# Performance work log

Hardware: AMD Instinct MI355X
Metric: run time of the kernel (lower is better)

## Reference

```python
import jax, jax.numpy as jnp
import numpy as np

D_MODEL = 768
NUM_HEADS = 12
HEAD_DIM = D_MODEL // NUM_HEADS

def setup_inputs() -> dict:
    key = jax.random.key(0)
    ks = jax.random.split(key, 7)
    B, S = 2, 4096
    q = jax.random.normal(ks[0], (B, S, D_MODEL), dtype=jnp.float32)
    k = jax.random.normal(ks[1], (B, S, D_MODEL), dtype=jnp.float32)
    v = jax.random.normal(ks[2], (B, S, D_MODEL), dtype=jnp.float32)
    # nn.Linear(d, d, bias=False): weight [out, in], y = x @ W.T
    s = 1.0 / np.sqrt(D_MODEL)
    W_q = jax.random.uniform(ks[3], (D_MODEL, D_MODEL), jnp.float32, -s, s)
    W_k = jax.random.uniform(ks[4], (D_MODEL, D_MODEL), jnp.float32, -s, s)
    W_v = jax.random.uniform(ks[5], (D_MODEL, D_MODEL), jnp.float32, -s, s)
    W_o = jax.random.uniform(ks[6], (D_MODEL, D_MODEL), jnp.float32, -s, s)
    return {"query": q, "key": k, "value": v,
            "W_q": W_q, "W_k": W_k, "W_v": W_v, "W_o": W_o}

def reference(query, key, value, W_q, W_k, W_v, W_o):
    B, S, _ = query.shape
    H, Dh = NUM_HEADS, HEAD_DIM
    scale = np.sqrt(Dh).astype(np.float32)

    def proj(x, W):  # x [B,S,D] -> [B,H,S,Dh]
        y = jnp.einsum('bsd,ed->bse', x, W)
        return y.reshape(B, S, H, Dh).transpose(0, 2, 1, 3)

    Q = proj(query, W_q)
    K = proj(key, W_k)
    V = proj(value, W_v)
    scores = jnp.einsum('bhqd,bhkd->bhqk', Q, K) / scale
    attn = jax.nn.softmax(scores, axis=-1)  # dropout p=0 -> identity (eval)
    out = jnp.einsum('bhqk,bhkd->bhqd', attn, V)
    out = out.transpose(0, 2, 1, 3).reshape(B, S, H * Dh)
    return jnp.einsum('bsd,ed->bse', out, W_o)
```

## Files before the change

### kernel.cpp

```cpp
#include <hip/hip_runtime.h>

#define D_MODEL 768
#define S_LEN   4096
#define NHEAD   12
#define HDIM    64
#define BATCH   2
#define M_ROWS  (BATCH * S_LEN)

typedef __bf16    bf16x8 __attribute__((ext_vector_type(8)));
typedef float     f32x4  __attribute__((ext_vector_type(4)));
typedef float     f32x16 __attribute__((ext_vector_type(16)));
typedef unsigned  u32x4  __attribute__((ext_vector_type(4)));

#define QSCALE 0.18033688011f

__device__ __forceinline__ unsigned int bfb(float x) {
    return (unsigned int)__builtin_bit_cast(unsigned short, (__bf16)x);
}

__device__ __forceinline__ unsigned cvtpk(float lo, float hi) {
    unsigned r;
    asm("v_cvt_pk_bf16_f32 %0, %1, %2" : "=v"(r) : "v"(lo), "v"(hi));
    return r;
}

#if !__has_builtin(__builtin_amdgcn_exp2f)
extern "C" __device__ float __ocml_native_exp2_f32(float);
#endif
__device__ __forceinline__ float fexp2(float x) {
#if __has_builtin(__builtin_amdgcn_exp2f)
    return __builtin_amdgcn_exp2f(x);
#else
    return __ocml_native_exp2_f32(x);
#endif
}

__device__ __forceinline__ void gload16(const void* g, const void* l) {
    __builtin_amdgcn_global_load_lds(
        (const __attribute__((address_space(1))) unsigned int*)g,
        (__attribute__((address_space(3))) unsigned int*)l, 16, 0, 0);
}

#define MFMA16(a, b, c) __builtin_amdgcn_mfma_f32_16x16x32_bf16(a, b, c, 0, 0, 0)
#define MFMA32(a, b, c) __builtin_amdgcn_mfma_f32_32x32x16_bf16(a, b, c, 0, 0, 0)

__global__ __launch_bounds__(256)
void cvt_bf16(const float* __restrict__ s0, const float* __restrict__ s1,
              const float* __restrict__ s2, const float* __restrict__ s3,
              __bf16* __restrict__ d0, __bf16* __restrict__ d1,
              __bf16* __restrict__ d2, __bf16* __restrict__ d3, int n) {
    const int z = blockIdx.y;
    const float* s = z == 0 ? s0 : z == 1 ? s1 : z == 2 ? s2 : s3;
    __bf16*      d = z == 0 ? d0 : z == 1 ? d1 : z == 2 ? d2 : d3;
    const size_t i = ((size_t)blockIdx.x * 256 + threadIdx.x) * 8;
    if (i >= (size_t)n) return;
    float4 a = *(const float4*)(s + i);
    float4 b = *(const float4*)(s + i + 4);
    bf16x8 o;
    o[0] = (__bf16)a.x; o[1] = (__bf16)a.y; o[2] = (__bf16)a.z; o[3] = (__bf16)a.w;
    o[4] = (__bf16)b.x; o[5] = (__bf16)b.y; o[6] = (__bf16)b.z; o[7] = (__bf16)b.w;
    *(bf16x8*)(d + i) = o;
}

__global__ __launch_bounds__(256)
void mm_qkv(const __bf16* __restrict__ X0, const __bf16* __restrict__ X1,
            const __bf16* __restrict__ X2, const __bf16* __restrict__ W0,
            const __bf16* __restrict__ W1, const __bf16* __restrict__ W2,
            __bf16* __restrict__ C0q, __bf16* __restrict__ C1k,
            __bf16* __restrict__ C2v) {
    __shared__ __align__(16) char lds[24576];
    const int z = blockIdx.z;
    const __bf16* Xb = z == 0 ? X0 : z == 1 ? X1 : X2;
    const __bf16* Wb = z == 0 ? W0 : z == 1 ? W1 : W2;

    const int t    = threadIdx.x;
    const int w    = t >> 6;
    const int wr   = w >> 1, wc = w & 1;
    const int lane = t & 63;
    const int q15  = lane & 15;
    const int g    = lane >> 4;
    const int n0   = blockIdx.x * 64;
    const int m0   = blockIdx.y * 128;

    f32x4 acc[4][2];
#pragma unroll
    for (int i = 0; i < 4; i++)
#pragma unroll
        for (int j = 0; j < 2; j++) acc[i][j] = (f32x4){0.f, 0.f, 0.f, 0.f};

    const int crow = lane >> 3;
    const int xcol = ((lane & 7) ^ crow) << 3;

    for (int k0 = 0; k0 < D_MODEL; k0 += 64) {
        __syncthreads();
#pragma unroll
        for (int j = 0; j < 4; j++) {
            const int c = 4 * w + j;
            gload16(Xb + (size_t)(m0 + 8 * c + crow) * D_MODEL + k0 + xcol,
                    lds + c * 1024);
        }
#pragma unroll
        for (int j = 0; j < 2; j++) {
            const int c = 2 * w + j;
            gload16(Wb + (size_t)(n0 + 8 * c + crow) * D_MODEL + k0 + xcol,
                    lds + 16384 + c * 1024);
        }
        __syncthreads();

#pragma unroll
        for (int kc = 0; kc < 2; kc++) {
            bf16x8 xa[4], wf[2];
#pragma unroll
            for (int mi = 0; mi < 4; mi++) {
                const int r = wr * 64 + mi * 16 + q15;
                xa[mi] = *(const bf16x8*)(lds + r * 128 +
                    ((64 * kc + 16 * g) ^ ((r & 7) << 4)));
            }
#pragma unroll
            for (int nj = 0; nj < 2; nj++) {
                const int r = wc * 32 + nj * 16 + q15;
                wf[nj] = *(const bf16x8*)(lds + 16384 + r * 128 +
                    ((64 * kc + 16 * g) ^ ((r & 7) << 4)));
            }
#pragma unroll
            for (int mi = 0; mi < 4; mi++)
#pragma unroll
                for (int nj = 0; nj < 2; nj++)
                    acc[mi][nj] = MFMA16(xa[mi], wf[nj], acc[mi][nj]);
        }
    }

#pragma unroll
    for (int mi = 0; mi < 4; mi++) {
#pragma unroll
        for (int nj = 0; nj < 2; nj++) {
            const int n  = n0 + wc * 32 + nj * 16 + q15;
            const int mb = m0 + wr * 64 + mi * 16 + 4 * g;
            const int h = n >> 6, dh = n & 63;
            if (z == 0) {
#pragma unroll
                for (int r = 0; r < 4; r++) {
                    const int m = mb + r, b = m >> 12, s = m & 4095;
                    C0q[(((size_t)(b * NHEAD + h)) * S_LEN + s) * HDIM + dh] =
                        (__bf16)(acc[mi][nj][r] * QSCALE);
                }
            } else if (z == 1) {
#pragma unroll
                for (int r = 0; r < 4; r++) {
                    const int m = mb + r, b = m >> 12, s = m & 4095;
                    C1k[(((size_t)(b * NHEAD + h)) * S_LEN + s) * HDIM + dh] =
                        (__bf16)acc[mi][nj][r];
                }
            } else {
                const int b = mb >> 12, s = mb & 4095;
                uint2 pk;
                pk.x = bfb(acc[mi][nj][0]) | (bfb(acc[mi][nj][1]) << 16);
                pk.y = bfb(acc[mi][nj][2]) | (bfb(acc[mi][nj][3]) << 16);
                *(uint2*)(C2v +
                    (((size_t)(b * NHEAD + h)) * HDIM + dh) * S_LEN + s) = pk;
            }
        }
    }
}

__global__ __launch_bounds__(256)
void mm_out(const __bf16* __restrict__ Xb, const __bf16* __restrict__ Wb,
            float* __restrict__ C0) {
    __shared__ __align__(16) char lds[24576];
    const int t    = threadIdx.x;
    const int w    = t >> 6;
    const int wr   = w >> 1, wc = w & 1;
    const int lane = t & 63;
    const int q15  = lane & 15;
    const int g    = lane >> 4;
    const int n0   = blockIdx.x * 64;
    const int m0   = blockIdx.y * 128;

    f32x4 acc[4][2];
#pragma unroll
    for (int i = 0; i < 4; i++)
#pragma unroll
        for (int j = 0; j < 2; j++) acc[i][j] = (f32x4){0.f, 0.f, 0.f, 0.f};

    const int crow = lane >> 3;
    const int xcol = ((lane & 7) ^ crow) << 3;

    for (int k0 = 0; k0 < D_MODEL; k0 += 64) {
        __syncthreads();
#pragma unroll
        for (int j = 0; j < 4; j++) {
            const int c = 4 * w + j;
            gload16(Xb + (size_t)(m0 + 8 * c + crow) * D_MODEL + k0 + xcol,
                    lds + c * 1024);
        }
#pragma unroll
        for (int j = 0; j < 2; j++) {
            const int c = 2 * w + j;
            gload16(Wb + (size_t)(n0 + 8 * c + crow) * D_MODEL + k0 + xcol,
                    lds + 16384 + c * 1024);
        }
        __syncthreads();

#pragma unroll
        for (int kc = 0; kc < 2; kc++) {
            bf16x8 xa[4], wf[2];
#pragma unroll
            for (int mi = 0; mi < 4; mi++) {
                const int r = wr * 64 + mi * 16 + q15;
                xa[mi] = *(const bf16x8*)(lds + r * 128 +
                    ((64 * kc + 16 * g) ^ ((r & 7) << 4)));
            }
#pragma unroll
            for (int nj = 0; nj < 2; nj++) {
                const int r = wc * 32 + nj * 16 + q15;
                wf[nj] = *(const bf16x8*)(lds + 16384 + r * 128 +
                    ((64 * kc + 16 * g) ^ ((r & 7) << 4)));
            }
#pragma unroll
            for (int mi = 0; mi < 4; mi++)
#pragma unroll
                for (int nj = 0; nj < 2; nj++)
                    acc[mi][nj] = MFMA16(xa[mi], wf[nj], acc[mi][nj]);
        }
    }

#pragma unroll
    for (int mi = 0; mi < 4; mi++)
#pragma unroll
        for (int nj = 0; nj < 2; nj++) {
            const int n  = n0 + wc * 32 + nj * 16 + q15;
            const int mb = m0 + wr * 64 + mi * 16 + 4 * g;
#pragma unroll
            for (int r = 0; r < 4; r++)
                C0[(size_t)(mb + r) * D_MODEL + n] = acc[mi][nj][r];
        }
}

__global__ __launch_bounds__(256, 2)
void flash_attn(const __bf16* __restrict__ Qb, const char* __restrict__ Kb,
                const char* __restrict__ Vtb, __bf16* __restrict__ Ab) {
    __shared__ __align__(16) char lds[32768];
    const int t    = threadIdx.x;
    const int w    = t >> 6;
    const int lane = t & 63;
    const int q31  = lane & 31;
    const int hl   = lane >> 5;
    const int swz  = (q31 & 7) << 4;

    const int bid = blockIdx.x;
    const int sb  = (bid & 7) * 96 + (bid >> 3);
    const int bh  = sb >> 5;
    const int qi  = sb & 31;
    const int b   = bh / NHEAD, h = bh % NHEAD;
    const int q0  = qi * 128 + w * 32;

    const char* kbase = Kb  + (size_t)bh * (S_LEN * HDIM * 2);
    const char* vbase = Vtb + (size_t)bh * (HDIM * S_LEN * 2);

    bf16x8 qf[4];
#pragma unroll
    for (int kc = 0; kc < 4; kc++)
        qf[kc] = *(const bf16x8*)(Qb +
            ((size_t)bh * S_LEN + q0 + q31) * HDIM + kc * 16 + hl * 8);

    const bf16x8 onesv = __builtin_bit_cast(bf16x8,
        (u32x4){0x3F803F80u, 0x3F803F80u, 0x3F803F80u, 0x3F803F80u});

    f32x16 o[2], ol;
#pragma unroll
    for (int mt = 0; mt < 2; mt++)
#pragma unroll
        for (int r = 0; r < 16; r++) o[mt][r] = 0.f;
#pragma unroll
    for (int r = 0; r < 16; r++) ol[r] = 0.f;

    const int crow = lane >> 3;
    const int scb  = ((lane & 7) << 4) ^ (crow << 4);

#define STAGE(BASE, KT)                                                        \
    {                                                                          \
        _Pragma("unroll")                                                      \
        for (int j = 0; j < 2; j++) {                                          \
            const int c = 2 * w + j;                                           \
            gload16(kbase + (size_t)((KT) * 64 + c * 8 + crow) * 128 + scb,    \
                    (BASE) + c * 1024);                                        \
            gload16(vbase + (size_t)(c * 8 + crow) * (S_LEN * 2) +             \
                        (size_t)(KT) * 128 + scb,                              \
                    (BASE) + 8192 + c * 1024);                                 \
        }                                                                      \
    }

#define COMPUTE(BASE)                                                          \
    {                                                                          \
        const char* Kt = (BASE);                                               \
        const char* Vt = (BASE) + 8192;                                        \
        f32x16 sA[2];                                                          \
        _Pragma("unroll")                                                      \
        for (int mt = 0; mt < 2; mt++)                                         \
            _Pragma("unroll")                                                  \
            for (int r = 0; r < 16; r++) sA[mt][r] = 0.f;                      \
        __builtin_amdgcn_s_setprio(1);                                         \
        _Pragma("unroll")                                                      \
        for (int kc = 0; kc < 4; kc++) {                                       \
            bf16x8 kf0 = *(const bf16x8*)(Kt + q31 * 128 +                     \
                                          ((32 * kc + 16 * hl) ^ swz));        \
            bf16x8 kf1 = *(const bf16x8*)(Kt + (32 + q31) * 128 +              \
                                          ((32 * kc + 16 * hl) ^ swz));        \
            sA[0] = MFMA32(kf0, qf[kc], sA[0]);                                \
            sA[1] = MFMA32(kf1, qf[kc], sA[1]);                                \
        }                                                                      \
        __builtin_amdgcn_s_setprio(0);                                         \
        _Pragma("unroll")                                                      \
        for (int mt = 0; mt < 2; mt++)                                         \
            _Pragma("unroll")                                                  \
            for (int r = 0; r < 16; r++) sA[mt][r] = fexp2(sA[mt][r]);         \
        u32x4 pf[4];                                                           \
        _Pragma("unroll")                                                      \
        for (int mt = 0; mt < 2; mt++)                                         \
            _Pragma("unroll")                                                  \
            for (int kvc = 0; kvc < 2; kvc++) {                                \
                unsigned w0 = cvtpk(sA[mt][8*kvc+0], sA[mt][8*kvc+1]);         \
                unsigned w1 = cvtpk(sA[mt][8*kvc+2], sA[mt][8*kvc+3]);         \
                unsigned w2 = cvtpk(sA[mt][8*kvc+4], sA[mt][8*kvc+5]);         \
                unsigned w3 = cvtpk(sA[mt][8*kvc+6], sA[mt][8*kvc+7]);         \
                asm volatile("v_permlane32_swap_b32 %0, %1"                    \
                             : "+v"(w0), "+v"(w2));                            \
                asm volatile("v_permlane32_swap_b32 %0, %1"                    \
                             : "+v"(w1), "+v"(w3));                            \
                pf[mt * 2 + kvc] = (u32x4){w0, w1, w2, w3};                    \
            }                                                                  \
        __builtin_amdgcn_s_setprio(1);                                         \
        _Pragma("unroll")                                                      \
        for (int ks = 0; ks < 4; ks++)                                         \
            ol = MFMA32(onesv, __builtin_bit_cast(bf16x8, pf[ks]), ol);        \
        _Pragma("unroll")                                                      \
        for (int mtd = 0; mtd < 2; mtd++)                                      \
            _Pragma("unroll")                                                  \
            for (int ks = 0; ks < 4; ks++) {                                   \
                bf16x8 vf = *(const bf16x8*)(Vt + (32 * mtd + q31) * 128 +     \
                                             ((32 * ks + 16 * hl) ^ swz));     \
                o[mtd] = MFMA32(vf,                                            \
                    __builtin_bit_cast(bf16x8, pf[ks]), o[mtd]);               \
            }                                                                  \
        __builtin_amdgcn_s_setprio(0);                                         \
    }

    STAGE(lds, 0);
    __syncthreads();
#pragma unroll 1
    for (int kt = 0; kt < S_LEN / 64; kt += 2) {
        STAGE(lds + 16384, kt + 1);
        COMPUTE(lds);
        __syncthreads();
        if (kt + 2 < S_LEN / 64) STAGE(lds, kt + 2);
        COMPUTE(lds + 16384);
        __syncthreads();
    }
#undef STAGE
#undef COMPUTE

    const float inv  = 1.0f / ol[0];
    const int   qrow = q0 + q31;
    __bf16* orow = Ab + ((size_t)b * S_LEN + qrow) * D_MODEL + h * HDIM;
#pragma unroll
    for (int mtd = 0; mtd < 2; mtd++)
#pragma unroll
        for (int rg = 0; rg < 4; rg++) {
            const int d0 = 32 * mtd + 8 * rg + 4 * hl;
            uint2 pk;
            pk.x = cvtpk(o[mtd][rg * 4 + 0] * inv, o[mtd][rg * 4 + 1] * inv);
            pk.y = cvtpk(o[mtd][rg * 4 + 2] * inv, o[mtd][rg * 4 + 3] * inv);
            *(uint2*)(orow + d0) = pk;
        }
}

extern "C" void kernel_launch(void* const* d_in, const int* in_sizes, int n_in,
                              void* d_out, int out_size, void* d_ws, size_t ws_size,
                              hipStream_t stream) {
    const float* q  = (const float*)d_in[0];
    const float* k  = (const float*)d_in[1];
    const float* v  = (const float*)d_in[2];
    const float* Wq = (const float*)d_in[3];
    const float* Wk = (const float*)d_in[4];
    const float* Wv = (const float*)d_in[5];
    const float* Wo = (const float*)d_in[6];
    float* out = (float*)d_out;

    const size_t per = (size_t)M_ROWS * D_MODEL;
    const size_t wsz = (size_t)D_MODEL * D_MODEL;
    __bf16* ws  = (__bf16*)d_ws;
    __bf16* qb  = ws;
    __bf16* kb  = qb  + per;
    __bf16* vb  = kb  + per;
    __bf16* Wqb = vb  + per;
    __bf16* Wkb = Wqb + wsz;
    __bf16* Wvb = Wkb + wsz;
    __bf16* Wob = Wvb + wsz;
    __bf16* Qhi = Wob + wsz;
    __bf16* Kbb = Qhi + per;
    __bf16* Vtb = Kbb + per;

    cvt_bf16<<<dim3((int)(per / 2048), 3), 256, 0, stream>>>(
        q, k, v, nullptr, qb, kb, vb, nullptr, (int)per);
    cvt_bf16<<<dim3((int)(wsz / 2048), 4), 256, 0, stream>>>(
        Wq, Wk, Wv, Wo, Wqb, Wkb, Wvb, Wob, (int)wsz);

    dim3 mmg(D_MODEL / 64, M_ROWS / 128, 3);
    mm_qkv<<<mmg, 256, 0, stream>>>(qb, kb, vb, Wqb, Wkb, Wvb, Qhi, Kbb, Vtb);

    flash_attn<<<768, 256, 0, stream>>>(Qhi, (const char*)Kbb,
                                        (const char*)Vtb, qb );

    dim3 mmo(D_MODEL / 64, M_ROWS / 128);
    mm_out<<<mmo, 256, 0, stream>>>(qb, Wob, out);
}
```

Before: 214.9 us.

## Split attention waves over query and key halves, reduce partials via LDS

Each wave now owns 64 query rows and half of every 64-key tile, so each K and V fragment read from LDS feeds two MFMAs instead of one. The row-sum MFMA against a ones vector is replaced by VALU summation of the exponentials plus a cross-half shuffle. The two key-half partial outputs and sums are combined through LDS at the end. Launch bounds rise to 3 blocks per CU, which tightens the register budget against the now larger per-wave accumulator state and may cause spills.

```diff
diff --git a/kernel.cpp b/kernel.cpp
--- a/kernel.cpp
+++ b/kernel.cpp
@@ -236,12 +236,14 @@
         }
 }
 
-__global__ __launch_bounds__(256, 2)
+__global__ __launch_bounds__(256, 3)
 void flash_attn(const __bf16* __restrict__ Qb, const char* __restrict__ Kb,
                 const char* __restrict__ Vtb, __bf16* __restrict__ Ab) {
-    __shared__ __align__(16) char lds[32768];
+    __shared__ __align__(16) char lds[33792];
     const int t    = threadIdx.x;
     const int w    = t >> 6;
+    const int qh   = w >> 1;
+    const int kh   = w & 1;
     const int lane = t & 63;
     const int q31  = lane & 31;
     const int hl   = lane >> 5;
@@ -252,27 +254,28 @@
     const int bh  = sb >> 5;
     const int qi  = sb & 31;
     const int b   = bh / NHEAD, h = bh % NHEAD;
-    const int q0  = qi * 128 + w * 32;
+    const int q0  = qi * 128;
 
     const char* kbase = Kb  + (size_t)bh * (S_LEN * HDIM * 2);
     const char* vbase = Vtb + (size_t)bh * (HDIM * S_LEN * 2);
 
-    bf16x8 qf[4];
-#pragma unroll
-    for (int kc = 0; kc < 4; kc++)
-        qf[kc] = *(const bf16x8*)(Qb +
-            ((size_t)bh * S_LEN + q0 + q31) * HDIM + kc * 16 + hl * 8);
-
-    const bf16x8 onesv = __builtin_bit_cast(bf16x8,
-        (u32x4){0x3F803F80u, 0x3F803F80u, 0x3F803F80u, 0x3F803F80u});
-
-    f32x16 o[2], ol;
-#pragma unroll
-    for (int mt = 0; mt < 2; mt++)
-#pragma unroll
-        for (int r = 0; r < 16; r++) o[mt][r] = 0.f;
-#pragma unroll
-    for (int r = 0; r < 16; r++) ol[r] = 0.f;
+    bf16x8 qf[2][4];
+#pragma unroll
+    for (int qb = 0; qb < 2; qb++)
+#pragma unroll
+        for (int kc = 0; kc < 4; kc++)
+            qf[qb][kc] = *(const bf16x8*)(Qb +
+                ((size_t)bh * S_LEN + q0 + 64 * qh + 32 * qb + q31) * HDIM +
+                kc * 16 + hl * 8);
+
+    f32x16 o[2][2];
+#pragma unroll
+    for (int qb = 0; qb < 2; qb++)
+#pragma unroll
+        for (int mtd = 0; mtd < 2; mtd++)
+#pragma unroll
+            for (int r = 0; r < 16; r++) o[qb][mtd][r] = 0.f;
+    float lrun[2] = {0.f, 0.f};
 
     const int crow = lane >> 3;
     const int scb  = ((lane & 7) << 4) ^ (crow << 4);
@@ -296,51 +299,61 @@
         const char* Vt = (BASE) + 8192;                                        \
         f32x16 sA[2];                                                          \
         _Pragma("unroll")                                                      \
-        for (int mt = 0; mt < 2; mt++)                                         \
+        for (int qb = 0; qb < 2; qb++)                                         \
             _Pragma("unroll")                                                  \
-            for (int r = 0; r < 16; r++) sA[mt][r] = 0.f;                      \
+            for (int r = 0; r < 16; r++) sA[qb][r] = 0.f;                      \
         __builtin_amdgcn_s_setprio(1);                                         \
         _Pragma("unroll")                                                      \
         for (int kc = 0; kc < 4; kc++) {                                       \
-            bf16x8 kf0 = *(const bf16x8*)(Kt + q31 * 128 +                     \
-                                          ((32 * kc + 16 * hl) ^ swz));        \
-            bf16x8 kf1 = *(const bf16x8*)(Kt + (32 + q31) * 128 +              \
-                                          ((32 * kc + 16 * hl) ^ swz));        \
-            sA[0] = MFMA32(kf0, qf[kc], sA[0]);                                \
-            sA[1] = MFMA32(kf1, qf[kc], sA[1]);                                \
+            bf16x8 kf = *(const bf16x8*)(Kt + (32 * kh + q31) * 128 +          \
+                                         ((32 * kc + 16 * hl) ^ swz));         \
+            sA[0] = MFMA32(kf, qf[0][kc], sA[0]);                              \
+            sA[1] = MFMA32(kf, qf[1][kc], sA[1]);                              \
         }                                                                      \
         __builtin_amdgcn_s_setprio(0);                                         \
         _Pragma("unroll")                                                      \
-        for (int mt = 0; mt < 2; mt++)                                         \
+        for (int qb = 0; qb < 2; qb++) {                                       \
+            float p0 = 0.f, p1 = 0.f, p2 = 0.f, p3 = 0.f;                      \
             _Pragma("unroll")                                                  \
-            for (int r = 0; r < 16; r++) sA[mt][r] = fexp2(sA[mt][r]);         \
-        u32x4 pf[4];                                                           \
-        _Pragma("unroll")                                                      \
-        for (int mt = 0; mt < 2; mt++)                                         \
+            for (int r = 0; r < 16; r += 4) {                                  \
+                const float e0 = fexp2(sA[qb][r + 0]);                         \
+                const float e1 = fexp2(sA[qb][r + 1]);                         \
+                const float e2 = fexp2(sA[qb][r + 2]);                         \
+                const float e3 = fexp2(sA[qb][r + 3]);                         \
+                sA[qb][r + 0] = e0; sA[qb][r + 1] = e1;                        \
+                sA[qb][r + 2] = e2; sA[qb][r + 3] = e3;                        \
+                p0 += e0; p1 += e1; p2 += e2; p3 += e3;                        \
+            }                                                                  \
+            float ps = (p0 + p1) + (p2 + p3);                                  \
+            ps += __shfl_xor(ps, 32);                                          \
+            lrun[qb] += ps;                                                    \
+        }                                                                      \
+        u32x4 pf[2][2];                                                        \
+        _Pragma("unroll")                                                      \
+        for (int qb = 0; qb < 2; qb++)                                         \
             _Pragma("unroll")                                                  \
             for (int kvc = 0; kvc < 2; kvc++) {                                \
-                unsigned w0 = cvtpk(sA[mt][8*kvc+0], sA[mt][8*kvc+1]);         \
-                unsigned w1 = cvtpk(sA[mt][8*kvc+2], sA[mt][8*kvc+3]);         \
-                unsigned w2 = cvtpk(sA[mt][8*kvc+4], sA[mt][8*kvc+5]);         \
-                unsigned w3 = cvtpk(sA[mt][8*kvc+6], sA[mt][8*kvc+7]);         \
+                unsigned w0 = cvtpk(sA[qb][8*kvc+0], sA[qb][8*kvc+1]);         \
+                unsigned w1 = cvtpk(sA[qb][8*kvc+2], sA[qb][8*kvc+3]);         \
+                unsigned w2 = cvtpk(sA[qb][8*kvc+4], sA[qb][8*kvc+5]);         \
+                unsigned w3 = cvtpk(sA[qb][8*kvc+6], sA[qb][8*kvc+7]);         \
                 asm volatile("v_permlane32_swap_b32 %0, %1"                    \
                              : "+v"(w0), "+v"(w2));                            \
                 asm volatile("v_permlane32_swap_b32 %0, %1"                    \
                              : "+v"(w1), "+v"(w3));                            \
-                pf[mt * 2 + kvc] = (u32x4){w0, w1, w2, w3};                    \
+                pf[qb][kvc] = (u32x4){w0, w1, w2, w3};                         \
             }                                                                  \
         __builtin_amdgcn_s_setprio(1);                                         \
         _Pragma("unroll")                                                      \
-        for (int ks = 0; ks < 4; ks++)                                         \
-            ol = MFMA32(onesv, __builtin_bit_cast(bf16x8, pf[ks]), ol);        \
-        _Pragma("unroll")                                                      \
         for (int mtd = 0; mtd < 2; mtd++)                                      \
             _Pragma("unroll")                                                  \
-            for (int ks = 0; ks < 4; ks++) {                                   \
+            for (int ks = 0; ks < 2; ks++) {                                   \
                 bf16x8 vf = *(const bf16x8*)(Vt + (32 * mtd + q31) * 128 +     \
-                                             ((32 * ks + 16 * hl) ^ swz));     \
-                o[mtd] = MFMA32(vf,                                            \
-                    __builtin_bit_cast(bf16x8, pf[ks]), o[mtd]);               \
+                    ((64 * kh + 32 * ks + 16 * hl) ^ swz));                    \
+                o[0][mtd] = MFMA32(vf,                                         \
+                    __builtin_bit_cast(bf16x8, pf[0][ks]), o[0][mtd]);         \
+                o[1][mtd] = MFMA32(vf,                                         \
+                    __builtin_bit_cast(bf16x8, pf[1][ks]), o[1][mtd]);         \
             }                                                                  \
         __builtin_amdgcn_s_setprio(0);                                         \
     }
@@ -359,19 +372,57 @@
 #undef STAGE
 #undef COMPUTE
 
-    const float inv  = 1.0f / ol[0];
-    const int   qrow = q0 + q31;
-    __bf16* orow = Ab + ((size_t)b * S_LEN + qrow) * D_MODEL + h * HDIM;
-#pragma unroll
-    for (int mtd = 0; mtd < 2; mtd++)
-#pragma unroll
-        for (int rg = 0; rg < 4; rg++) {
-            const int d0 = 32 * mtd + 8 * rg + 4 * hl;
-            uint2 pk;
-            pk.x = cvtpk(o[mtd][rg * 4 + 0] * inv, o[mtd][rg * 4 + 1] * inv);
-            pk.y = cvtpk(o[mtd][rg * 4 + 2] * inv, o[mtd][rg * 4 + 3] * inv);
-            *(uint2*)(orow + d0) = pk;
-        }
+    __syncthreads();
+    if (kh == 1) {
+#pragma unroll
+        for (int qb = 0; qb < 2; qb++) {
+#pragma unroll
+            for (int mtd = 0; mtd < 2; mtd++)
+#pragma unroll
+                for (int rg = 0; rg < 4; rg++) {
+                    f32x4 v4;
+#pragma unroll
+                    for (int j = 0; j < 4; j++) v4[j] = o[qb][mtd][4 * rg + j];
+                    *(f32x4*)(lds + qh * 16384 + (qb * 2 + mtd) * 4096 +
+                              rg * 1024 + (hl * 32 + q31) * 16) = v4;
+                }
+            *(float*)(lds + 32768 + ((qh * 2 + qb) * 2 + hl) * 128 + q31 * 4) =
+                lrun[qb];
+        }
+    }
+    __syncthreads();
+    if (kh == 0) {
+#pragma unroll
+        for (int qb = 0; qb < 2; qb++) {
+            lrun[qb] += *(const float*)(lds + 32768 +
+                ((qh * 2 + qb) * 2 + hl) * 128 + q31 * 4);
+#pragma unroll
+            for (int mtd = 0; mtd < 2; mtd++)
+#pragma unroll
+                for (int rg = 0; rg < 4; rg++) {
+                    f32x4 pp = *(const f32x4*)(lds + qh * 16384 +
+                        (qb * 2 + mtd) * 4096 + rg * 1024 +
+                        (hl * 32 + q31) * 16);
+#pragma unroll
+                    for (int j = 0; j < 4; j++) o[qb][mtd][4 * rg + j] += pp[j];
+                }
+            const float inv  = 1.0f / lrun[qb];
+            const int   qrow = q0 + 64 * qh + 32 * qb + q31;
+            __bf16* orow = Ab + ((size_t)b * S_LEN + qrow) * D_MODEL + h * HDIM;
+#pragma unroll
+            for (int mtd = 0; mtd < 2; mtd++)
+#pragma unroll
+                for (int rg = 0; rg < 4; rg++) {
+                    const int d0 = 32 * mtd + 8 * rg + 4 * hl;
+                    uint2 pk;
+                    pk.x = cvtpk(o[qb][mtd][rg * 4 + 0] * inv,
+                                 o[qb][mtd][rg * 4 + 1] * inv);
+                    pk.y = cvtpk(o[qb][mtd][rg * 4 + 2] * inv,
+                                 o[qb][mtd][rg * 4 + 3] * inv);
+                    *(uint2*)(orow + d0) = pk;
+                }
+        }
+    }
 }
 
 extern "C" void kernel_launch(void* const* d_in, const int* in_sizes, int n_in,
```

Result: slower. 240.7 us (+12.0%).
